# Performance work log

Hardware: AMD Instinct MI355X
Metric: run time of the kernel (lower is better)

## Reference

```python
import jax, jax.numpy as jnp
import numpy as np

B, N, E, M, H, OUT, F = 4, 10000, 160000, 4, 64, 64, 64


def setup_inputs() -> dict:
    key = jax.random.key(0)
    k1, k2, k3, k4, k5, k6 = jax.random.split(key, 6)
    node_fts = jax.random.normal(k1, (B, N, M, H), dtype=jnp.float32)
    hidden = jax.random.normal(k2, (B, N, M, H), dtype=jnp.float32)
    edge_fts = jax.random.normal(k3, (B, E, F), dtype=jnp.float32)
    edge_indices = jax.random.randint(k4, (B, E, 2), 0, N, dtype=jnp.int64)
    # hk.Linear params (truncated-normal-ish init approximated by scaled normal)
    W_nh = jax.random.normal(k5, (2 * H, OUT), dtype=jnp.float32) / np.sqrt(2 * H)
    b_nh = jnp.zeros((OUT,), dtype=jnp.float32)
    W_e = jax.random.normal(k6, (F, 1), dtype=jnp.float32) / np.sqrt(F)
    b_e = jnp.zeros((1,), dtype=jnp.float32)
    return {"node_fts": node_fts, "hidden": hidden, "edge_fts": edge_fts,
            "W_nh": W_nh, "b_nh": b_nh, "W_e": W_e, "b_e": b_e,
            "edge_indices": edge_indices}


def reference(node_fts, hidden, edge_fts, W_nh, b_nh, W_e, b_e, edge_indices):
    nb_nodes = node_fts.shape[1]
    src = edge_indices[..., 0]  # [B, E]
    tgt = edge_indices[..., 1]  # [B, E]
    # fuse node and hidden features, project: [B, N, M, 2H] @ [2H, OUT]
    nh = jnp.concatenate([node_fts, hidden], axis=-1)
    nh_fts = jnp.einsum('bnmc,co->bnmo', nh, W_nh) + b_nh  # [B, N, M, OUT]
    # gather per-edge source-node features along node axis
    nh_values = jnp.take_along_axis(nh_fts, src[:, :, None, None], axis=1)  # [B, E, M, OUT]
    # scalar gate per edge
    edge_coeff = jnp.einsum('bef,fo->beo', edge_fts, W_e) + b_e  # [B, E, 1]
    filtered = edge_coeff[..., None] * nh_values  # [B, E, M, OUT]
    # scatter-sum messages to target nodes, per batch element
    seg = jax.vmap(lambda d, s: jax.ops.segment_sum(d, s, num_segments=nb_nodes))
    updated_bits = seg(filtered, tgt)  # [B, N, M, OUT]
    return updated_bits
```

## Files before the change

### kernel.cpp

```cpp
#include <hip/hip_runtime.h>

#define Bc 4
#define Nc 10000
#define Ec 160000
#define NSEG (Bc * Nc)
#define NEDGE (Bc * Ec)
#define CAP 64
#define PROJ_BLOCKS 1250
#define GATE_BLOCKS 1250

typedef __attribute__((ext_vector_type(8))) short bf16x8;
typedef __attribute__((ext_vector_type(4))) float f32x4;

__device__ __forceinline__ unsigned short f2bf(float f) {
    union { float f; unsigned u; } x; x.f = f;
    return (unsigned short)((x.u + 0x7FFFu + ((x.u >> 16) & 1u)) >> 16);
}
__device__ __forceinline__ float bfhi(unsigned u) {
    union { unsigned u; float f; } x; x.u = u & 0xFFFF0000u; return x.f;
}
__device__ __forceinline__ float bflo(unsigned u) {
    union { unsigned u; float f; } x; x.u = u << 16; return x.f;
}

__device__ __forceinline__ float reduce16(float* p, int lane) {
#pragma unroll
    for (int off = 1, n = 8; off < 16; off <<= 1, n >>= 1) {
        const bool hi2 = (lane & off) != 0;
#pragma unroll
        for (int i = 0; i < 8; ++i)
            if (i < n) {
                const float keep = hi2 ? p[2 * i + 1] : p[2 * i];
                const float send = hi2 ? p[2 * i] : p[2 * i + 1];
                p[i] = keep + __shfl_xor(send, off, 64);
            }
    }
    return p[0];
}

__global__ __launch_bounds__(256) void proj_kernel(
    const float* __restrict__ node, const float* __restrict__ hid,
    const float* __restrict__ Wnh, const float* __restrict__ bnh,
    unsigned short* __restrict__ nhf)
{
    __shared__ __align__(16) unsigned short wlds[8192];
    const int t = threadIdx.x;
    const int lane = t & 63;

#pragma unroll
    for (int i = 0; i < 4; ++i) {
        const int f    = t + 256 * i;
        const int kt   = f >> 8;
        const int ct   = (f >> 6) & 3;
        const int l    = f & 63;
        const int quad = l >> 4, m = l & 15;
        const int col  = 16 * ct + m;
        const int krow = quad * 8 + 32 * kt;
        bf16x8 fr;
#pragma unroll
        for (int j = 0; j < 8; ++j)
            fr[j] = (short)f2bf(Wnh[(size_t)(krow + j) * 64 + col]);
        *(bf16x8*)(wlds + (size_t)f * 8) = fr;
    }
    __syncthreads();

    const int wv   = (int)(blockIdx.x * 4 + (t >> 6));
    const int m    = lane & 15;
    const int quad = lane >> 4;

    float bias[4];
#pragma unroll
    for (int ct = 0; ct < 4; ++ct) bias[ct] = bnh[m + 16 * ct];

    float4 lo[2][4], hi[2][4];
#pragma unroll
    for (int half = 0; half < 2; ++half) {
        const int arow = (wv * 2 + half) * 16 + m;
#pragma unroll
        for (int kt = 0; kt < 4; ++kt) {
            const int kbase = quad * 8 + 32 * kt;
            const float* pp = (kbase < 64)
                ? (node + (size_t)arow * 64 + kbase)
                : (hid  + (size_t)arow * 64 + (kbase - 64));
            lo[half][kt] = *(const float4*)pp;
            hi[half][kt] = *(const float4*)(pp + 4);
        }
    }

#pragma unroll
    for (int half = 0; half < 2; ++half) {
        f32x4 acc[4];
#pragma unroll
        for (int ct = 0; ct < 4; ++ct) acc[ct] = (f32x4){0.f, 0.f, 0.f, 0.f};
#pragma unroll
        for (int kt = 0; kt < 4; ++kt) {
            bf16x8 a;
            a[0] = (short)f2bf(lo[half][kt].x); a[1] = (short)f2bf(lo[half][kt].y);
            a[2] = (short)f2bf(lo[half][kt].z); a[3] = (short)f2bf(lo[half][kt].w);
            a[4] = (short)f2bf(hi[half][kt].x); a[5] = (short)f2bf(hi[half][kt].y);
            a[6] = (short)f2bf(hi[half][kt].z); a[7] = (short)f2bf(hi[half][kt].w);
#pragma unroll
            for (int ct = 0; ct < 4; ++ct) {
                const bf16x8 bf = *(const bf16x8*)(wlds + (size_t)((kt * 4 + ct) * 64 + lane) * 8);
                acc[ct] = __builtin_amdgcn_mfma_f32_16x16x32_bf16(a, bf, acc[ct], 0, 0, 0);
            }
        }
        const int r0 = (wv * 2 + half) * 16 + quad * 4;
#pragma unroll
        for (int ct = 0; ct < 4; ++ct) {
            const int col = m + 16 * ct;
#pragma unroll
            for (int reg = 0; reg < 4; ++reg)
                nhf[(size_t)(r0 + reg) * 64 + col] = f2bf(acc[ct][reg] + bias[ct]);
        }
    }
}

__global__ __launch_bounds__(256) void gate_kernel(
    const float* __restrict__ efts, const int* __restrict__ eidx,
    const float* __restrict__ We, const float* __restrict__ be,
    int2* __restrict__ epair, int* __restrict__ cnt)
{
    const int lane = threadIdx.x & 63;
    const int w  = (int)(blockIdx.x * 4 + (threadIdx.x >> 6));
    const int e0 = w * 128;
    const int b  = e0 / Ec;
    const int cb = b * Nc;
    const float4 w4 = *(const float4*)(We + (size_t)(lane & 15) * 4);
    const float be0 = be[0];
    const int perm = 4 * (lane & 15) + (lane >> 4);

    float4 v[16];
    const float* base0 = efts + (size_t)e0 * 64;
#pragma unroll
    for (int j = 0; j < 16; ++j)
        v[j] = *(const float4*)(base0 + (size_t)j * 256 + lane * 4);
    const int2 st0 = *(const int2*)(eidx + (size_t)(e0 + perm) * 2);

    float p[16];
#pragma unroll
    for (int j = 0; j < 16; ++j)
        p[j] = v[j].x * w4.x + v[j].y * w4.y + v[j].z * w4.z + v[j].w * w4.w;

    const float* base1 = efts + (size_t)(e0 + 64) * 64;
#pragma unroll
    for (int j = 0; j < 16; ++j)
        v[j] = *(const float4*)(base1 + (size_t)j * 256 + lane * 4);
    const int2 st1 = *(const int2*)(eidx + (size_t)(e0 + 64 + perm) * 2);

    {
        const float cval = reduce16(p, lane) + be0;
        const int seg  = cb + st0.y;
        const int slot = atomicAdd(&cnt[seg], 1);
        if (slot < CAP)
            epair[(size_t)seg * 128 + slot] = make_int2(st0.x, __float_as_int(cval));
    }

#pragma unroll
    for (int j = 0; j < 16; ++j)
        p[j] = v[j].x * w4.x + v[j].y * w4.y + v[j].z * w4.z + v[j].w * w4.w;

    {
        const float cval = reduce16(p, lane) + be0;
        const int seg  = cb + st1.y;
        const int slot = atomicAdd(&cnt[seg], 1);
        if (slot < CAP)
            epair[(size_t)seg * 128 + slot] = make_int2(st1.x, __float_as_int(cval));
    }
}

__global__ __launch_bounds__(256) void gather_kernel(
    const int* __restrict__ cnt, const int2* epair,
    const unsigned* __restrict__ nhf, float* out)
{
    const int lane = threadIdx.x & 63;
    int seg = (int)((blockIdx.x * blockDim.x + threadIdx.x) >> 6);
    if (seg >= NSEG) return;
    seg = __builtin_amdgcn_readfirstlane(seg);
    const int b = seg / Nc;
    const int deg = cnt[seg];
    const int end = deg < CAP ? deg : CAP;
    const int2* bp = epair + (size_t)seg * 128;
    const unsigned* base = nhf + (size_t)b * Nc * 128 + lane * 2;
    const int2 my = bp[lane];

    f32x4 acc[4];
#pragma unroll
    for (int j = 0; j < 4; ++j) acc[j] = (f32x4){0.f, 0.f, 0.f, 0.f};

    int i = 0;
    for (; i + 8 <= end; i += 8) {
        int sx[8]; float cc[8]; uint2 r[8];
#pragma unroll
        for (int j = 0; j < 8; ++j) {
            sx[j] = __shfl(my.x, i + j, 64);
            cc[j] = __int_as_float(__shfl(my.y, i + j, 64));
        }
#pragma unroll
        for (int j = 0; j < 8; ++j) r[j] = *(const uint2*)(base + (size_t)sx[j] * 128);
#pragma unroll
        for (int j = 0; j < 8; ++j) {
            acc[j & 3][0] += cc[j] * bflo(r[j].x);
            acc[j & 3][1] += cc[j] * bfhi(r[j].x);
            acc[j & 3][2] += cc[j] * bflo(r[j].y);
            acc[j & 3][3] += cc[j] * bfhi(r[j].y);
        }
    }
    if (i + 4 <= end) {
        int sx[4]; float cc[4]; uint2 r[4];
#pragma unroll
        for (int j = 0; j < 4; ++j) {
            sx[j] = __shfl(my.x, i + j, 64);
            cc[j] = __int_as_float(__shfl(my.y, i + j, 64));
        }
#pragma unroll
        for (int j = 0; j < 4; ++j) r[j] = *(const uint2*)(base + (size_t)sx[j] * 128);
#pragma unroll
        for (int j = 0; j < 4; ++j) {
            acc[j][0] += cc[j] * bflo(r[j].x);
            acc[j][1] += cc[j] * bfhi(r[j].x);
            acc[j][2] += cc[j] * bflo(r[j].y);
            acc[j][3] += cc[j] * bfhi(r[j].y);
        }
        i += 4;
    }
    for (; i < end; ++i) {
        const int sx = __shfl(my.x, i, 64);
        const float cc = __int_as_float(__shfl(my.y, i, 64));
        const uint2 r = *(const uint2*)(base + (size_t)sx * 128);
        acc[0][0] += cc * bflo(r.x);
        acc[0][1] += cc * bfhi(r.x);
        acc[0][2] += cc * bflo(r.y);
        acc[0][3] += cc * bfhi(r.y);
    }
    float4 o;
    o.x = (acc[0][0] + acc[1][0]) + (acc[2][0] + acc[3][0]);
    o.y = (acc[0][1] + acc[1][1]) + (acc[2][1] + acc[3][1]);
    o.z = (acc[0][2] + acc[1][2]) + (acc[2][2] + acc[3][2]);
    o.w = (acc[0][3] + acc[1][3]) + (acc[2][3] + acc[3][3]);
    *(float4*)(out + (size_t)seg * 256 + lane * 4) = o;
}

__global__ __launch_bounds__(256) void edge_atomic_kernel(
    const float* __restrict__ efts, const int* __restrict__ eidx,
    const float* __restrict__ We, const float* __restrict__ be,
    const unsigned* __restrict__ nhf, float* __restrict__ out)
{
    const int lane = threadIdx.x & 63;
    const int eg   = (int)((blockIdx.x * blockDim.x + threadIdx.x) >> 6);
    if (eg >= NEDGE) return;
    const int b = eg / Ec;
    float c = efts[(size_t)eg * 64 + lane] * We[lane];
#pragma unroll
    for (int off = 32; off > 0; off >>= 1) c += __shfl_xor(c, off, 64);
    c += be[0];
    const int src = eidx[(size_t)eg * 2 + 0];
    const int tgt = eidx[(size_t)eg * 2 + 1];
    const uint2 r = *(const uint2*)(nhf + ((size_t)(b * Nc + src)) * 128 + lane * 2);
    float* op = out + ((size_t)(b * Nc + tgt)) * 256 + lane * 4;
    atomicAdd(op + 0, c * bflo(r.x));
    atomicAdd(op + 1, c * bfhi(r.x));
    atomicAdd(op + 2, c * bflo(r.y));
    atomicAdd(op + 3, c * bfhi(r.y));
}

extern "C" void kernel_launch(void* const* d_in, const int* in_sizes, int n_in,
                              void* d_out, int out_size, void* d_ws, size_t ws_size,
                              hipStream_t stream) {
    const float* node = (const float*)d_in[0];
    const float* hid  = (const float*)d_in[1];
    const float* efts = (const float*)d_in[2];
    const float* Wnh  = (const float*)d_in[3];
    const float* bnh  = (const float*)d_in[4];
    const float* We   = (const float*)d_in[5];
    const float* be   = (const float*)d_in[6];
    const int*   eidx = (const int*)d_in[7];
    float* out = (float*)d_out;

    unsigned* ws = (unsigned*)d_ws;
    unsigned short* nhf16 = (unsigned short*)ws;
    int* cnt = (int*)(ws + 5120000);
    const size_t ws_needed = (size_t)5160000 * 4;

    if (ws_size >= ws_needed) {
        int2* epair = (int2*)d_out;
        hipMemsetAsync(cnt, 0, (size_t)NSEG * sizeof(int), stream);
        proj_kernel<<<PROJ_BLOCKS, 256, 0, stream>>>(node, hid, Wnh, bnh, nhf16);
        gate_kernel<<<GATE_BLOCKS, 256, 0, stream>>>(efts, eidx, We, be, epair, cnt);
        gather_kernel<<<NSEG / 4, 256, 0, stream>>>(cnt, epair, (const unsigned*)ws, out);
    } else {
        proj_kernel<<<PROJ_BLOCKS, 256, 0, stream>>>(node, hid, Wnh, bnh, nhf16);
        hipMemsetAsync(d_out, 0, (size_t)out_size * sizeof(float), stream);
        edge_atomic_kernel<<<NEDGE / 4, 256, 0, stream>>>(efts, eidx, We, be, (const unsigned*)ws, out);
    }
}
```

Baseline: 351.9 us.

## Merge projection and gate kernels into one launch, compact edge-pair buffer in workspace

The projection and edge-gate kernels are merged into one launch, with blocks split by index, so the two independent stages run concurrently and one launch is saved. When the workspace is large enough, the edge-pair buffer moves out of the output into the workspace with a 64-slot stride instead of 128, which halves its footprint. The per-target atomic slot reservations are also issued before the feature loads so their latency overlaps. The merged kernel carries both code paths and their combined register use, which may lower occupancy.

```diff
diff --git a/kernel.cpp b/kernel.cpp
--- a/kernel.cpp
+++ b/kernel.cpp
@@ -38,139 +38,137 @@
     return p[0];
 }
 
-__global__ __launch_bounds__(256) void proj_kernel(
+__global__ __launch_bounds__(256) void proj_gate_kernel(
     const float* __restrict__ node, const float* __restrict__ hid,
     const float* __restrict__ Wnh, const float* __restrict__ bnh,
-    unsigned short* __restrict__ nhf)
+    unsigned short* __restrict__ nhf,
+    const float* __restrict__ efts, const int* __restrict__ eidx,
+    const float* __restrict__ We, const float* __restrict__ be,
+    int2* __restrict__ epair, int slot_stride, int* __restrict__ cnt)
 {
     __shared__ __align__(16) unsigned short wlds[8192];
     const int t = threadIdx.x;
     const int lane = t & 63;
 
-#pragma unroll
-    for (int i = 0; i < 4; ++i) {
-        const int f    = t + 256 * i;
-        const int kt   = f >> 8;
-        const int ct   = (f >> 6) & 3;
-        const int l    = f & 63;
-        const int quad = l >> 4, m = l & 15;
-        const int col  = 16 * ct + m;
-        const int krow = quad * 8 + 32 * kt;
-        bf16x8 fr;
-#pragma unroll
-        for (int j = 0; j < 8; ++j)
-            fr[j] = (short)f2bf(Wnh[(size_t)(krow + j) * 64 + col]);
-        *(bf16x8*)(wlds + (size_t)f * 8) = fr;
-    }
-    __syncthreads();
-
-    const int wv   = (int)(blockIdx.x * 4 + (t >> 6));
-    const int m    = lane & 15;
-    const int quad = lane >> 4;
-
-    float bias[4];
-#pragma unroll
-    for (int ct = 0; ct < 4; ++ct) bias[ct] = bnh[m + 16 * ct];
-
-    float4 lo[2][4], hi[2][4];
-#pragma unroll
-    for (int half = 0; half < 2; ++half) {
-        const int arow = (wv * 2 + half) * 16 + m;
-#pragma unroll
-        for (int kt = 0; kt < 4; ++kt) {
-            const int kbase = quad * 8 + 32 * kt;
-            const float* pp = (kbase < 64)
-                ? (node + (size_t)arow * 64 + kbase)
-                : (hid  + (size_t)arow * 64 + (kbase - 64));
-            lo[half][kt] = *(const float4*)pp;
-            hi[half][kt] = *(const float4*)(pp + 4);
-        }
-    }
-
-#pragma unroll
-    for (int half = 0; half < 2; ++half) {
-        f32x4 acc[4];
-#pragma unroll
-        for (int ct = 0; ct < 4; ++ct) acc[ct] = (f32x4){0.f, 0.f, 0.f, 0.f};
-#pragma unroll
-        for (int kt = 0; kt < 4; ++kt) {
-            bf16x8 a;
-            a[0] = (short)f2bf(lo[half][kt].x); a[1] = (short)f2bf(lo[half][kt].y);
-            a[2] = (short)f2bf(lo[half][kt].z); a[3] = (short)f2bf(lo[half][kt].w);
-            a[4] = (short)f2bf(hi[half][kt].x); a[5] = (short)f2bf(hi[half][kt].y);
-            a[6] = (short)f2bf(hi[half][kt].z); a[7] = (short)f2bf(hi[half][kt].w);
+    if (blockIdx.x < PROJ_BLOCKS) {
+#pragma unroll
+        for (int i = 0; i < 4; ++i) {
+            const int f    = t + 256 * i;
+            const int kt   = f >> 8;
+            const int ct   = (f >> 6) & 3;
+            const int l    = f & 63;
+            const int quad = l >> 4, m = l & 15;
+            const int col  = 16 * ct + m;
+            const int krow = quad * 8 + 32 * kt;
+            bf16x8 fr;
+#pragma unroll
+            for (int j = 0; j < 8; ++j)
+                fr[j] = (short)f2bf(Wnh[(size_t)(krow + j) * 64 + col]);
+            *(bf16x8*)(wlds + (size_t)f * 8) = fr;
+        }
+        __syncthreads();
+
+        const int wv   = (int)(blockIdx.x * 4 + (t >> 6));
+        const int m    = lane & 15;
+        const int quad = lane >> 4;
+
+        float bias[4];
+#pragma unroll
+        for (int ct = 0; ct < 4; ++ct) bias[ct] = bnh[m + 16 * ct];
+
+        float4 lo[2][4], hi[2][4];
+#pragma unroll
+        for (int half = 0; half < 2; ++half) {
+            const int arow = (wv * 2 + half) * 16 + m;
+#pragma unroll
+            for (int kt = 0; kt < 4; ++kt) {
+                const int kbase = quad * 8 + 32 * kt;
+                const float* pp = (kbase < 64)
+                    ? (node + (size_t)arow * 64 + kbase)
+                    : (hid  + (size_t)arow * 64 + (kbase - 64));
+                lo[half][kt] = *(const float4*)pp;
+                hi[half][kt] = *(const float4*)(pp + 4);
+            }
+        }
+
+#pragma unroll
+        for (int half = 0; half < 2; ++half) {
+            f32x4 acc[4];
+#pragma unroll
+            for (int ct = 0; ct < 4; ++ct) acc[ct] = (f32x4){0.f, 0.f, 0.f, 0.f};
+#pragma unroll
+            for (int kt = 0; kt < 4; ++kt) {
+                bf16x8 a;
+                a[0] = (short)f2bf(lo[half][kt].x); a[1] = (short)f2bf(lo[half][kt].y);
+                a[2] = (short)f2bf(lo[half][kt].z); a[3] = (short)f2bf(lo[half][kt].w);
+                a[4] = (short)f2bf(hi[half][kt].x); a[5] = (short)f2bf(hi[half][kt].y);
+                a[6] = (short)f2bf(hi[half][kt].z); a[7] = (short)f2bf(hi[half][kt].w);
+#pragma unroll
+                for (int ct = 0; ct < 4; ++ct) {
+                    const bf16x8 bf = *(const bf16x8*)(wlds + (size_t)((kt * 4 + ct) * 64 + lane) * 8);
+                    acc[ct] = __builtin_amdgcn_mfma_f32_16x16x32_bf16(a, bf, acc[ct], 0, 0, 0);
+                }
+            }
+            const int r0 = (wv * 2 + half) * 16 + quad * 4;
 #pragma unroll
             for (int ct = 0; ct < 4; ++ct) {
-                const bf16x8 bf = *(const bf16x8*)(wlds + (size_t)((kt * 4 + ct) * 64 + lane) * 8);
-                acc[ct] = __builtin_amdgcn_mfma_f32_16x16x32_bf16(a, bf, acc[ct], 0, 0, 0);
+                const int col = m + 16 * ct;
+#pragma unroll
+                for (int reg = 0; reg < 4; ++reg)
+                    nhf[(size_t)(r0 + reg) * 64 + col] = f2bf(acc[ct][reg] + bias[ct]);
             }
         }
-        const int r0 = (wv * 2 + half) * 16 + quad * 4;
-#pragma unroll
-        for (int ct = 0; ct < 4; ++ct) {
-            const int col = m + 16 * ct;
-#pragma unroll
-            for (int reg = 0; reg < 4; ++reg)
-                nhf[(size_t)(r0 + reg) * 64 + col] = f2bf(acc[ct][reg] + bias[ct]);
-        }
-    }
-}
-
-__global__ __launch_bounds__(256) void gate_kernel(
-    const float* __restrict__ efts, const int* __restrict__ eidx,
-    const float* __restrict__ We, const float* __restrict__ be,
-    int2* __restrict__ epair, int* __restrict__ cnt)
-{
-    const int lane = threadIdx.x & 63;
-    const int w  = (int)(blockIdx.x * 4 + (threadIdx.x >> 6));
-    const int e0 = w * 128;
-    const int b  = e0 / Ec;
-    const int cb = b * Nc;
-    const float4 w4 = *(const float4*)(We + (size_t)(lane & 15) * 4);
-    const float be0 = be[0];
-    const int perm = 4 * (lane & 15) + (lane >> 4);
-
-    float4 v[16];
-    const float* base0 = efts + (size_t)e0 * 64;
-#pragma unroll
-    for (int j = 0; j < 16; ++j)
-        v[j] = *(const float4*)(base0 + (size_t)j * 256 + lane * 4);
-    const int2 st0 = *(const int2*)(eidx + (size_t)(e0 + perm) * 2);
-
-    float p[16];
-#pragma unroll
-    for (int j = 0; j < 16; ++j)
-        p[j] = v[j].x * w4.x + v[j].y * w4.y + v[j].z * w4.z + v[j].w * w4.w;
-
-    const float* base1 = efts + (size_t)(e0 + 64) * 64;
-#pragma unroll
-    for (int j = 0; j < 16; ++j)
-        v[j] = *(const float4*)(base1 + (size_t)j * 256 + lane * 4);
-    const int2 st1 = *(const int2*)(eidx + (size_t)(e0 + 64 + perm) * 2);
-
-    {
-        const float cval = reduce16(p, lane) + be0;
-        const int seg  = cb + st0.y;
-        const int slot = atomicAdd(&cnt[seg], 1);
-        if (slot < CAP)
-            epair[(size_t)seg * 128 + slot] = make_int2(st0.x, __float_as_int(cval));
-    }
-
-#pragma unroll
-    for (int j = 0; j < 16; ++j)
-        p[j] = v[j].x * w4.x + v[j].y * w4.y + v[j].z * w4.z + v[j].w * w4.w;
-
-    {
-        const float cval = reduce16(p, lane) + be0;
-        const int seg  = cb + st1.y;
-        const int slot = atomicAdd(&cnt[seg], 1);
-        if (slot < CAP)
-            epair[(size_t)seg * 128 + slot] = make_int2(st1.x, __float_as_int(cval));
+    } else {
+        const int w  = (int)((blockIdx.x - PROJ_BLOCKS) * 4 + (t >> 6));
+        const int e0 = w * 128;
+        const int b  = e0 / Ec;
+        const int cb = b * Nc;
+        const float4 w4 = *(const float4*)(We + (size_t)(lane & 15) * 4);
+        const float be0 = be[0];
+        const int perm = 4 * (lane & 15) + (lane >> 4);
+
+        const int2 st0 = *(const int2*)(eidx + (size_t)(e0 + perm) * 2);
+        const int2 st1 = *(const int2*)(eidx + (size_t)(e0 + 64 + perm) * 2);
+        const int seg0 = cb + st0.y;
+        const int seg1 = cb + st1.y;
+        const int slot0 = atomicAdd(&cnt[seg0], 1);
+        const int slot1 = atomicAdd(&cnt[seg1], 1);
+
+        float4 v[16];
+        const float* base0 = efts + (size_t)e0 * 64;
+#pragma unroll
+        for (int j = 0; j < 16; ++j)
+            v[j] = *(const float4*)(base0 + (size_t)j * 256 + lane * 4);
+        float p[16];
+#pragma unroll
+        for (int j = 0; j < 16; ++j)
+            p[j] = v[j].x * w4.x + v[j].y * w4.y + v[j].z * w4.z + v[j].w * w4.w;
+
+        const float* base1 = efts + (size_t)(e0 + 64) * 64;
+#pragma unroll
+        for (int j = 0; j < 16; ++j)
+            v[j] = *(const float4*)(base1 + (size_t)j * 256 + lane * 4);
+
+        {
+            const float cval = reduce16(p, lane) + be0;
+            if (slot0 < CAP)
+                epair[(size_t)seg0 * slot_stride + slot0] = make_int2(st0.x, __float_as_int(cval));
+        }
+
+#pragma unroll
+        for (int j = 0; j < 16; ++j)
+            p[j] = v[j].x * w4.x + v[j].y * w4.y + v[j].z * w4.z + v[j].w * w4.w;
+
+        {
+            const float cval = reduce16(p, lane) + be0;
+            if (slot1 < CAP)
+                epair[(size_t)seg1 * slot_stride + slot1] = make_int2(st1.x, __float_as_int(cval));
+        }
     }
 }
 
 __global__ __launch_bounds__(256) void gather_kernel(
-    const int* __restrict__ cnt, const int2* epair,
+    const int* __restrict__ cnt, const int2* epair, int slot_stride,
     const unsigned* __restrict__ nhf, float* out)
 {
     const int lane = threadIdx.x & 63;
@@ -180,7 +178,7 @@
     const int b = seg / Nc;
     const int deg = cnt[seg];
     const int end = deg < CAP ? deg : CAP;
-    const int2* bp = epair + (size_t)seg * 128;
+    const int2* bp = epair + (size_t)seg * slot_stride;
     const unsigned* base = nhf + (size_t)b * Nc * 128 + lane * 2;
     const int2 my = bp[lane];
 
@@ -280,16 +278,22 @@
     unsigned* ws = (unsigned*)d_ws;
     unsigned short* nhf16 = (unsigned short*)ws;
     int* cnt = (int*)(ws + 5120000);
-    const size_t ws_needed = (size_t)5160000 * 4;
-
-    if (ws_size >= ws_needed) {
-        int2* epair = (int2*)d_out;
+    const size_t ws_compact = (size_t)10280000 * 4;
+    const size_t ws_minimal = (size_t)5160000 * 4;
+
+    if (ws_size >= ws_minimal) {
+        int2* epair;
+        int stride;
+        if (ws_size >= ws_compact) { epair = (int2*)(ws + 5160000); stride = 64; }
+        else                       { epair = (int2*)d_out;          stride = 128; }
         hipMemsetAsync(cnt, 0, (size_t)NSEG * sizeof(int), stream);
-        proj_kernel<<<PROJ_BLOCKS, 256, 0, stream>>>(node, hid, Wnh, bnh, nhf16);
-        gate_kernel<<<GATE_BLOCKS, 256, 0, stream>>>(efts, eidx, We, be, epair, cnt);
-        gather_kernel<<<NSEG / 4, 256, 0, stream>>>(cnt, epair, (const unsigned*)ws, out);
+        proj_gate_kernel<<<PROJ_BLOCKS + GATE_BLOCKS, 256, 0, stream>>>(
+            node, hid, Wnh, bnh, nhf16, efts, eidx, We, be, epair, stride, cnt);
+        gather_kernel<<<NSEG / 4, 256, 0, stream>>>(cnt, epair, stride, (const unsigned*)ws, out);
     } else {
-        proj_kernel<<<PROJ_BLOCKS, 256, 0, stream>>>(node, hid, Wnh, bnh, nhf16);
+        proj_gate_kernel<<<PROJ_BLOCKS, 256, 0, stream>>>(
+            node, hid, Wnh, bnh, nhf16, efts, eidx, We, be,
+            (int2*)d_out , 128, (int*)d_out );
         hipMemsetAsync(d_out, 0, (size_t)out_size * sizeof(float), stream);
         edge_atomic_kernel<<<NEDGE / 4, 256, 0, stream>>>(efts, eidx, We, be, (const unsigned*)ws, out);
     }
```

Measured after the change: 348.6 us. About the same (-0.9%).
